# Kernel optimization log

Measured on AMD Instinct MI355X. Metric: run time of the kernel, lower is better.

## Reference

```python
import jax, jax.numpy as jnp
import numpy as np


def setup_inputs() -> dict:
    key = jax.random.key(0)
    k0, k1, k2, k3 = jax.random.split(key, 4)
    B, L, D, H = 8, 4096, 300, 128  # batch, leaves (power of 2), embed dim, hidden
    x = jax.random.normal(k0, (B, L, D), jnp.float32)
    W_leaf = jax.random.normal(k1, (D, 2 * H), jnp.float32) * (1.0 / np.sqrt(D))
    b_leaf = jnp.zeros((2 * H,), jnp.float32)
    W_l = jax.random.normal(k2, (H, 5 * H), jnp.float32) * (1.0 / np.sqrt(H))
    W_r = jax.random.normal(k3, (H, 5 * H), jnp.float32) * (1.0 / np.sqrt(H))
    b = jnp.zeros((5 * H,), jnp.float32)
    return {"x": x, "W_leaf": W_leaf, "b_leaf": b_leaf, "W_l": W_l, "W_r": W_r, "b": b}


def reference(x, W_leaf, b_leaf, W_l, W_r, b):
    """Binary TreeLSTM over a complete tree: leaves -> root.

    x: [B, L, D] leaf embeddings, L a power of 2.
    Leaf transform: linear projection split into (h, c) (SPINN-style).
    REDUCE: 5-gate child-sum-of-two composition.
    Returns root hidden state: [B, H].
    """
    H = W_l.shape[0]
    hc = x @ W_leaf + b_leaf                     # [B, L, 2H]
    h, c = hc[..., :H], hc[..., H:]
    levels = int(np.log2(x.shape[1]))
    for _ in range(levels):                      # level-batched tree reduction
        h_l, h_r = h[:, 0::2], h[:, 1::2]        # [B, n/2, H]
        c_l, c_r = c[:, 0::2], c[:, 1::2]
        gates = h_l @ W_l + h_r @ W_r + b        # [B, n/2, 5H]
        i, fl, fr, o, g = jnp.split(gates, 5, axis=-1)
        c = (jax.nn.sigmoid(fl) * c_l
             + jax.nn.sigmoid(fr) * c_r
             + jax.nn.sigmoid(i) * jnp.tanh(g))
        h = jax.nn.sigmoid(o) * jnp.tanh(c)
    return h[:, 0]                               # root hidden state [B, H]
```

## Files before the change

kernel.cpp:

```cpp
#include <hip/hip_runtime.h>
#include <hip/hip_bf16.h>
#include <math.h>


typedef __attribute__((ext_vector_type(8))) short bfrag8;
typedef __attribute__((ext_vector_type(4))) float f32x4;

__device__ __forceinline__ float rcpf(float x) { return __builtin_amdgcn_rcpf(x); }
__device__ __forceinline__ float sigf(float x) { return rcpf(1.0f + __expf(-x)); }
__device__ __forceinline__ float tanh_f(float x) {
    float e = __expf(2.0f * x);
    return 1.0f - 2.0f * rcpf(e + 1.0f);
}
__device__ __forceinline__ short f2bf(float f) {
    __hip_bfloat16 h = __float2bfloat16(f);
    return *reinterpret_cast<short*>(&h);
}
__device__ __forceinline__ float bf2f(short s) {
    union { unsigned int u; float f; } v;
    v.u = ((unsigned int)(unsigned short)s) << 16;
    return v.f;
}
__device__ __forceinline__ bfrag8 pack8(f32x4 a, f32x4 b) {
    union { int i[4]; bfrag8 v; } u;
    asm("v_cvt_pk_bf16_f32 %0, %1, %2" : "=v"(u.i[0]) : "v"(a[0]), "v"(a[1]));
    asm("v_cvt_pk_bf16_f32 %0, %1, %2" : "=v"(u.i[1]) : "v"(a[2]), "v"(a[3]));
    asm("v_cvt_pk_bf16_f32 %0, %1, %2" : "=v"(u.i[2]) : "v"(b[0]), "v"(b[1]));
    asm("v_cvt_pk_bf16_f32 %0, %1, %2" : "=v"(u.i[3]) : "v"(b[2]), "v"(b[3]));
    return u.v;
}
#define GLDS(gp, lp) __builtin_amdgcn_global_load_lds( \
    (const __attribute__((address_space(1))) void*)(gp), \
    (__attribute__((address_space(3))) void*)(lp), 16, 0, 0)

__global__ __launch_bounds__(256) void leaf_kernel(
    const float* __restrict__ x,     const float* __restrict__ Wleaf,
    const float* __restrict__ W_l,   const float* __restrict__ W_r,
    const float* __restrict__ bleaf,
    short* __restrict__ hD,
    short* __restrict__ cDb,
    short* __restrict__ Wcat_ch)
{
    __shared__ float Als[128 * 64];
    __shared__ short Bls[8 * 256 * 8];
    const int tid  = threadIdx.x;
    const int w    = tid >> 6, lane = tid & 63;
    const int quad = lane >> 4, l16 = lane & 15;
    const int mBlk = blockIdx.x * 128;
    const int waveM = (w >> 1) * 64, waveN = (w & 1) * 64;

    if (blockIdx.x < 160) {
        #pragma unroll
        for (int e = 0; e < 4; ++e) {
            int idx = blockIdx.x * 1024 + e * 256 + tid;
            int n = idx >> 8, k = idx & 255;
            float v = (k < 128) ? W_l[k * 640 + n] : W_r[(k - 128) * 640 + n];
            Wcat_ch[(((size_t)(k >> 3)) * 640 + n) * 8 + (k & 7)] = f2bf(v);
        }
    }

    f32x4 acc[2][4][4] = {};
    const f32x4 zero4 = {0.f, 0.f, 0.f, 0.f};

    for (int c = 0; c < 5; ++c) {
        const int k0c = c * 64;
        {
            const int q_lds = lane & 15;
            const int rsub  = lane >> 4;
            #pragma unroll
            for (int g = 0; g < 8; ++g) {
                int row = w * 32 + g * 4 + rsub;
                int q_g = (q_lds & 8) | ((q_lds & 7) ^ (row & 7));
                if (c < 4 || q_g < 11) {
                    GLDS(x + (size_t)(mBlk + row) * 300 + k0c + q_g * 4,
                         (char*)Als + (w * 32 + g * 4) * 256);
                } else {
                    *(f32x4*)((char*)Als + row * 256 + q_lds * 16) = zero4;
                }
            }
        }
        #pragma unroll
        for (int uu = 0; uu < 8; ++uu) {
            int ccl = uu, nl = tid;
            int k0  = (c * 8 + ccl) * 8;
            f32x4 v0, v1;
            #pragma unroll
            for (int jj = 0; jj < 4; ++jj)
                v0[jj] = (k0 + jj < 300) ? Wleaf[(size_t)(k0 + jj) * 256 + nl] : 0.0f;
            #pragma unroll
            for (int jj = 0; jj < 4; ++jj)
                v1[jj] = (k0 + 4 + jj < 300) ? Wleaf[(size_t)(k0 + 4 + jj) * 256 + nl] : 0.0f;
            *(bfrag8*)(Bls + (ccl * 256 + nl) * 8) = pack8(v0, v1);
        }
        __syncthreads();
        #pragma unroll
        for (int ks = 0; ks < 2; ++ks) {
            const int ca = ks * 4 + quad;
            bfrag8 af[4];
            #pragma unroll
            for (int i = 0; i < 4; ++i) {
                int r  = waveM + i * 16 + l16;
                int u0 = 2 * ca, u1 = 2 * ca + 1;
                int s0 = (u0 & 8) | ((u0 & 7) ^ (r & 7));
                int s1 = (u1 & 8) | ((u1 & 7) ^ (r & 7));
                f32x4 a0 = *(const f32x4*)(Als + r * 64 + s0 * 4);
                f32x4 a1 = *(const f32x4*)(Als + r * 64 + s1 * 4);
                af[i] = pack8(a0, a1);
            }
            #pragma unroll
            for (int nh = 0; nh < 2; ++nh) {
                bfrag8 bf4[4];
                #pragma unroll
                for (int jn = 0; jn < 4; ++jn)
                    bf4[jn] = *(const bfrag8*)(Bls + (ca * 256 + nh * 128
                                                      + waveN + jn * 16 + l16) * 8);
                #pragma unroll
                for (int i = 0; i < 4; ++i)
                    #pragma unroll
                    for (int jn = 0; jn < 4; ++jn)
                        acc[nh][i][jn] = __builtin_amdgcn_mfma_f32_16x16x32_bf16(
                                             af[i], bf4[jn], acc[nh][i][jn], 0, 0, 0);
            }
        }
        __syncthreads();
    }

    #pragma unroll
    for (int nh = 0; nh < 2; ++nh) {
        #pragma unroll
        for (int i = 0; i < 4; ++i) {
            int row0 = mBlk + waveM + i * 16 + quad * 4;
            #pragma unroll
            for (int jn = 0; jn < 4; ++jn) {
                int col = nh * 128 + waveN + jn * 16 + l16;
                float bv = bleaf[col];
                #pragma unroll
                for (int rg = 0; rg < 4; ++rg) {
                    float v = acc[nh][i][jn][rg] + bv;
                    int m = row0 + rg;
                    if (nh == 0) {
                        int hc = col;
                        hD[(((size_t)((m & 1) * 16 + (hc >> 3))) * 16384 + (m >> 1)) * 8
                           + (hc & 7)] = f2bf(v);
                    } else {
                        int ch = col - 128;
                        cDb[(size_t)(ch >> 4) * 32768 * 16 + (size_t)m * 16 + (ch & 15)]
                            = f2bf(v);
                    }
                }
            }
        }
    }
}

template<int CIN_BF, int COUT_BF>
__global__ __launch_bounds__(256, 2) void level_ws_t(
    const short* __restrict__ A,
    const void*  __restrict__ cprev,
    const short* __restrict__ Wch,
    const float* __restrict__ bias,
    short* __restrict__ hout, void* __restrict__ cout_,
    int M, int nst)
{
    __shared__ short Als[32 * 64 * 8];
    const int tid  = threadIdx.x;
    const int w    = tid >> 6, lane = tid & 63;
    const int quad = lane >> 4, l16 = lane & 15;
    const int j   = blockIdx.y;
    const int tb0 = blockIdx.x * 64 * nst;
    const int h   = j * 16 + l16;

    #pragma unroll
    for (int s = 0; s < 8; ++s)
        GLDS(A + ((size_t)(s * 4 + w) * M + tb0 + lane) * 8,
             (char*)Als + (s * 4 + w) * 1024);

    bfrag8 Wfr[5][8];
    #pragma unroll
    for (int g = 0; g < 5; ++g)
        #pragma unroll
        for (int s = 0; s < 8; ++s)
            Wfr[g][s] = *(const bfrag8*)(Wch + ((size_t)(s * 4 + quad) * 640
                                                + g * 128 + h) * 8);
    const float bi  = bias[h],       bfl = bias[128 + h], bfr_ = bias[256 + h];
    const float bo  = bias[384 + h], bg  = bias[512 + h];

    const int Mn = M >> 1;
    for (int st = 0; st < nst; ++st) {
        const int tb = tb0 + st * 64;
        __syncthreads();

        f32x4 acc[5] = {};
        #pragma unroll
        for (int s = 0; s < 8; ++s) {
            bfrag8 af = *(const bfrag8*)(Als + ((s * 4 + quad) * 64 + w * 16 + l16) * 8);
            #pragma unroll
            for (int g = 0; g < 5; ++g)
                acc[g] = __builtin_amdgcn_mfma_f32_16x16x32_bf16(af, Wfr[g][s], acc[g], 0, 0, 0);
        }

        if (st + 1 < nst) {
            __syncthreads();
            #pragma unroll
            for (int s = 0; s < 8; ++s)
                GLDS(A + ((size_t)(s * 4 + w) * M + tb + 64 + lane) * 8,
                     (char*)Als + (s * 4 + w) * 1024);
        }

        #pragma unroll
        for (int rg = 0; rg < 4; ++rg) {
            int m = tb + w * 16 + quad * 4 + rg;
            float gi  = acc[0][rg] + bi;
            float gfl = acc[1][rg] + bfl;
            float gfr = acc[2][rg] + bfr_;
            float go  = acc[3][rg] + bo;
            float gg  = acc[4][rg] + bg;
            float cl, cr;
            if (CIN_BF) {
                const short* cp = (const short*)cprev;
                size_t base = (size_t)(h >> 4) * ((size_t)2 * M) * 16
                              + (size_t)(2 * m) * 16 + (h & 15);
                cl = bf2f(cp[base]);
                cr = bf2f(cp[base + 16]);
            } else {
                const float* cp = (const float*)cprev;
                cl = cp[(size_t)(2 * m) * 128 + h];
                cr = cp[(size_t)(2 * m + 1) * 128 + h];
            }
            float cn  = sigf(gfl) * cl + sigf(gfr) * cr + sigf(gi) * tanh_f(gg);
            float hn  = sigf(go) * tanh_f(cn);
            hout[(((size_t)((m & 1) * 16 + (h >> 3))) * Mn + (m >> 1)) * 8
                 + (h & 7)] = f2bf(hn);
            if (COUT_BF) {
                ((short*)cout_)[(size_t)(h >> 4) * (size_t)M * 16
                                + (size_t)m * 16 + (h & 15)] = f2bf(cn);
            } else {
                ((float*)cout_)[(size_t)m * 128 + h] = cn;
            }
        }
    }
}

__global__ __launch_bounds__(512) void finish_kernel(
    const short* __restrict__ hin,
    const float* __restrict__ cin,
    const short* __restrict__ Wch, const float* __restrict__ bias,
    float* __restrict__ out)
{
    __shared__ short hP[32 * 64 * 8];
    __shared__ short hQ[32 * 32 * 8];
    __shared__ float cA[128 * 128];
    __shared__ float cB[64 * 128];
    const int tid  = threadIdx.x;
    const int w    = tid >> 6, lane = tid & 63;
    const int quad = lane >> 4, l16 = lane & 15;
    const int h    = w * 16 + l16;

    #pragma unroll
    for (int g = 0; g < 4; ++g)
        GLDS(hin + ((size_t)((g * 8 + w) * 64 + lane)) * 8,
             (char*)hP + ((g * 8 + w) * 64) * 16);
    #pragma unroll
    for (int g = 0; g < 8; ++g)
        GLDS(cin + ((size_t)((g * 8 + w) * 64 + lane)) * 4,
             (char*)cA + ((g * 8 + w) * 64) * 16);

    bfrag8 Wfr[5][8];
    #pragma unroll
    for (int g = 0; g < 5; ++g)
        #pragma unroll
        for (int s = 0; s < 8; ++s)
            Wfr[g][s] = *(const bfrag8*)(Wch + ((size_t)(s * 4 + quad) * 640
                                                + g * 128 + h) * 8);
    const float bi  = bias[h],       bfl = bias[128 + h], bfr_ = bias[256 + h];
    const float bo  = bias[384 + h], bg  = bias[512 + h];

    __syncthreads();

    #pragma unroll
    for (int t = 0; t < 4; ++t) {
        const int Mo = 64 >> t;
        const short* hsrc = (t & 1) ? hQ : hP;
        short* hdst       = (t & 1) ? hP : hQ;
        const float* cread  = (t & 1) ? cB : cA;
        float*       cwrite = (t & 1) ? cA : cB;
        const int nrt = (Mo + 15) >> 4;

        for (int rt = 0; rt < nrt; ++rt) {
            f32x4 acc[5] = {};
            #pragma unroll
            for (int s = 0; s < 8; ++s) {
                bfrag8 af = *(const bfrag8*)(hsrc + ((s * 4 + quad) * Mo
                                                     + rt * 16 + l16) * 8);
                #pragma unroll
                for (int g = 0; g < 5; ++g)
                    acc[g] = __builtin_amdgcn_mfma_f32_16x16x32_bf16(
                                 af, Wfr[g][s], acc[g], 0, 0, 0);
            }
            #pragma unroll
            for (int rg = 0; rg < 4; ++rg) {
                int m = rt * 16 + quad * 4 + rg;
                if (m < Mo) {
                    float gi  = acc[0][rg] + bi;
                    float gfl = acc[1][rg] + bfl;
                    float gfr = acc[2][rg] + bfr_;
                    float go  = acc[3][rg] + bo;
                    float gg  = acc[4][rg] + bg;
                    float cl  = cread[(2 * m) * 128 + h];
                    float cr  = cread[(2 * m + 1) * 128 + h];
                    float cn  = sigf(gfl) * cl + sigf(gfr) * cr + sigf(gi) * tanh_f(gg);
                    float hn  = sigf(go) * tanh_f(cn);
                    if (t == 3) {
                        out[(size_t)m * 128 + h] = hn;
                    } else {
                        hdst[(((m & 1) * 16 + (h >> 3)) * (Mo >> 1) + (m >> 1)) * 8
                             + (h & 7)] = f2bf(hn);
                        cwrite[m * 128 + h] = cn;
                    }
                }
            }
        }
        __syncthreads();
    }
}

extern "C" void kernel_launch(void* const* d_in, const int* in_sizes, int n_in,
                              void* d_out, int out_size, void* d_ws, size_t ws_size,
                              hipStream_t stream)
{
    const float* x      = (const float*)d_in[0];
    const float* W_leaf = (const float*)d_in[1];
    const float* b_leaf = (const float*)d_in[2];
    const float* W_l    = (const float*)d_in[3];
    const float* W_r    = (const float*)d_in[4];
    const float* b      = (const float*)d_in[5];
    float* out = (float*)d_out;

    char* p = (char*)d_ws;
    short* hA    = (short*)p; p += (size_t)32 * 16384 * 16 + 1024;
    short* hB    = (short*)p; p += (size_t)32 * 8192 * 16 + 1024;
    char*  c0    = p;         p += (size_t)32768 * 128 * 4;
    char*  c1    = p;         p += (size_t)16384 * 128 * 4;
    short* WcatC = (short*)p; p += (size_t)32 * 640 * 16;

    leaf_kernel<<<256, 256, 0, stream>>>(
        x, W_leaf, W_l, W_r, b_leaf, hA, (short*)c0, WcatC);

    level_ws_t<1, 1><<<dim3(16384 / 256, 8), 256, 0, stream>>>(
        hA, c0, WcatC, b, hB, c1, 16384, 4);
    level_ws_t<1, 0><<<dim3(8192 / 128, 8), 256, 0, stream>>>(
        hB, c1, WcatC, b, hA, c0, 8192, 2);

    const short* hin = hA; const char* cin = c0;
    int M = 4096;
    for (int lev = 3; lev <= 8; ++lev) {
        short* ho = (lev & 1) ? hB : hA;
        char*  co = (lev & 1) ? c1 : c0;
        int nst = (lev == 3) ? 2 : 1;
        level_ws_t<0, 0><<<dim3(M / (64 * nst), 8), 256, 0, stream>>>(
            hin, cin, WcatC, b, ho, co, M, nst);
        hin = ho; cin = co;
        M >>= 1;
    }

    finish_kernel<<<1, 512, 0, stream>>>(hA, (const float*)c0, WcatC, b, out);
}
```

Measured before the change: 167.3 us.

## Pre-convert leaf weights to bf16 in separate kernel and halve leaf tile

Adds a reorder kernel that converts W_l/W_r and W_leaf into bf16 chunked layouts once, instead of every leaf block re-reading fp32 W_leaf with strided scalar loads and converting it. The leaf kernel now streams the pre-packed B tile with async global-to-LDS loads, uses 64-row M tiles with each wave owning 64 columns, and runs 512 blocks for better occupancy. This costs an extra kernel launch and less reuse of each B tile across rows.

Result: no change. 166.2 us (-0.6%).

```diff
diff --git a/kernel.cpp b/kernel.cpp
--- a/kernel.cpp
+++ b/kernel.cpp
@@ -33,33 +33,41 @@
     (const __attribute__((address_space(1))) void*)(gp), \
     (__attribute__((address_space(3))) void*)(lp), 16, 0, 0)
 
+__global__ __launch_bounds__(256) void reorder_kernel(
+    const float* __restrict__ W_l, const float* __restrict__ W_r,
+    const float* __restrict__ W_leaf,
+    short* __restrict__ Wcat_ch, short* __restrict__ Wleaf_ch)
+{
+    int idx = blockIdx.x * 256 + threadIdx.x;
+    if (idx < 163840) {
+        int n = idx >> 8, k = idx & 255;
+        float v = (k < 128) ? W_l[k * 640 + n] : W_r[(k - 128) * 640 + n];
+        Wcat_ch[(((size_t)(k >> 3)) * 640 + n) * 8 + (k & 7)] = f2bf(v);
+        return;
+    }
+    idx -= 163840;
+    if (idx < 81920) {
+        int n = idx / 320, k = idx - n * 320;
+        short v = (k < 300) ? f2bf(W_leaf[k * 256 + n]) : (short)0;
+        Wleaf_ch[(((size_t)(k >> 3)) * 256 + n) * 8 + (k & 7)] = v;
+    }
+}
+
 __global__ __launch_bounds__(256) void leaf_kernel(
-    const float* __restrict__ x,     const float* __restrict__ Wleaf,
-    const float* __restrict__ W_l,   const float* __restrict__ W_r,
+    const float* __restrict__ x,   const short* __restrict__ Bw,
     const float* __restrict__ bleaf,
     short* __restrict__ hD,
-    short* __restrict__ cDb,
-    short* __restrict__ Wcat_ch)
-{
-    __shared__ float Als[128 * 64];
+    short* __restrict__ cDb)
+{
+    __shared__ float Als[64 * 64];
     __shared__ short Bls[8 * 256 * 8];
     const int tid  = threadIdx.x;
     const int w    = tid >> 6, lane = tid & 63;
     const int quad = lane >> 4, l16 = lane & 15;
-    const int mBlk = blockIdx.x * 128;
-    const int waveM = (w >> 1) * 64, waveN = (w & 1) * 64;
-
-    if (blockIdx.x < 160) {
-        #pragma unroll
-        for (int e = 0; e < 4; ++e) {
-            int idx = blockIdx.x * 1024 + e * 256 + tid;
-            int n = idx >> 8, k = idx & 255;
-            float v = (k < 128) ? W_l[k * 640 + n] : W_r[(k - 128) * 640 + n];
-            Wcat_ch[(((size_t)(k >> 3)) * 640 + n) * 8 + (k & 7)] = f2bf(v);
-        }
-    }
-
-    f32x4 acc[2][4][4] = {};
+    const int mBlk = blockIdx.x * 64;
+    const int waveN = w * 64;
+
+    f32x4 acc[4][4] = {};
     const f32x4 zero4 = {0.f, 0.f, 0.f, 0.f};
 
     for (int c = 0; c < 5; ++c) {
@@ -68,38 +76,32 @@
             const int q_lds = lane & 15;
             const int rsub  = lane >> 4;
             #pragma unroll
-            for (int g = 0; g < 8; ++g) {
-                int row = w * 32 + g * 4 + rsub;
+            for (int g = 0; g < 4; ++g) {
+                int row = w * 16 + g * 4 + rsub;
                 int q_g = (q_lds & 8) | ((q_lds & 7) ^ (row & 7));
                 if (c < 4 || q_g < 11) {
                     GLDS(x + (size_t)(mBlk + row) * 300 + k0c + q_g * 4,
-                         (char*)Als + (w * 32 + g * 4) * 256);
+                         (char*)Als + (w * 16 + g * 4) * 256);
                 } else {
                     *(f32x4*)((char*)Als + row * 256 + q_lds * 16) = zero4;
                 }
             }
         }
         #pragma unroll
-        for (int uu = 0; uu < 8; ++uu) {
-            int ccl = uu, nl = tid;
-            int k0  = (c * 8 + ccl) * 8;
-            f32x4 v0, v1;
-            #pragma unroll
-            for (int jj = 0; jj < 4; ++jj)
-                v0[jj] = (k0 + jj < 300) ? Wleaf[(size_t)(k0 + jj) * 256 + nl] : 0.0f;
-            #pragma unroll
-            for (int jj = 0; jj < 4; ++jj)
-                v1[jj] = (k0 + 4 + jj < 300) ? Wleaf[(size_t)(k0 + 4 + jj) * 256 + nl] : 0.0f;
-            *(bfrag8*)(Bls + (ccl * 256 + nl) * 8) = pack8(v0, v1);
+        for (int g = 0; g < 8; ++g) {
+            int i   = w * 8 + g;
+            int cc  = i >> 2, colg = (i & 3) * 64;
+            GLDS(Bw + ((size_t)(c * 8 + cc) * 256 + colg + lane) * 8,
+                 (char*)Bls + ((cc * 256 + colg)) * 16);
         }
         __syncthreads();
         #pragma unroll
         for (int ks = 0; ks < 2; ++ks) {
             const int ca = ks * 4 + quad;
-            bfrag8 af[4];
+            bfrag8 af[4], bf4[4];
             #pragma unroll
             for (int i = 0; i < 4; ++i) {
-                int r  = waveM + i * 16 + l16;
+                int r  = i * 16 + l16;
                 int u0 = 2 * ca, u1 = 2 * ca + 1;
                 int s0 = (u0 & 8) | ((u0 & 7) ^ (r & 7));
                 int s1 = (u1 & 8) | ((u1 & 7) ^ (r & 7));
@@ -108,45 +110,37 @@
                 af[i] = pack8(a0, a1);
             }
             #pragma unroll
-            for (int nh = 0; nh < 2; ++nh) {
-                bfrag8 bf4[4];
+            for (int jn = 0; jn < 4; ++jn)
+                bf4[jn] = *(const bfrag8*)(Bls + (ca * 256 + waveN + jn * 16 + l16) * 8);
+            #pragma unroll
+            for (int i = 0; i < 4; ++i)
                 #pragma unroll
                 for (int jn = 0; jn < 4; ++jn)
-                    bf4[jn] = *(const bfrag8*)(Bls + (ca * 256 + nh * 128
-                                                      + waveN + jn * 16 + l16) * 8);
-                #pragma unroll
-                for (int i = 0; i < 4; ++i)
-                    #pragma unroll
-                    for (int jn = 0; jn < 4; ++jn)
-                        acc[nh][i][jn] = __builtin_amdgcn_mfma_f32_16x16x32_bf16(
-                                             af[i], bf4[jn], acc[nh][i][jn], 0, 0, 0);
-            }
+                    acc[i][jn] = __builtin_amdgcn_mfma_f32_16x16x32_bf16(
+                                     af[i], bf4[jn], acc[i][jn], 0, 0, 0);
         }
         __syncthreads();
     }
 
     #pragma unroll
-    for (int nh = 0; nh < 2; ++nh) {
-        #pragma unroll
-        for (int i = 0; i < 4; ++i) {
-            int row0 = mBlk + waveM + i * 16 + quad * 4;
-            #pragma unroll
-            for (int jn = 0; jn < 4; ++jn) {
-                int col = nh * 128 + waveN + jn * 16 + l16;
-                float bv = bleaf[col];
-                #pragma unroll
-                for (int rg = 0; rg < 4; ++rg) {
-                    float v = acc[nh][i][jn][rg] + bv;
-                    int m = row0 + rg;
-                    if (nh == 0) {
-                        int hc = col;
-                        hD[(((size_t)((m & 1) * 16 + (hc >> 3))) * 16384 + (m >> 1)) * 8
-                           + (hc & 7)] = f2bf(v);
-                    } else {
-                        int ch = col - 128;
-                        cDb[(size_t)(ch >> 4) * 32768 * 16 + (size_t)m * 16 + (ch & 15)]
-                            = f2bf(v);
-                    }
+    for (int i = 0; i < 4; ++i) {
+        int row0 = mBlk + i * 16 + quad * 4;
+        #pragma unroll
+        for (int jn = 0; jn < 4; ++jn) {
+            int col = waveN + jn * 16 + l16;
+            float bv = bleaf[col];
+            #pragma unroll
+            for (int rg = 0; rg < 4; ++rg) {
+                float v = acc[i][jn][rg] + bv;
+                int m = row0 + rg;
+                if (col < 128) {
+                    int hc = col;
+                    hD[(((size_t)((m & 1) * 16 + (hc >> 3))) * 16384 + (m >> 1)) * 8
+                       + (hc & 7)] = f2bf(v);
+                } else {
+                    int ch = col - 128;
+                    cDb[(size_t)(ch >> 4) * 32768 * 16 + (size_t)m * 16 + (ch & 15)]
+                        = f2bf(v);
                 }
             }
         }
@@ -342,9 +336,11 @@
     char*  c0    = p;         p += (size_t)32768 * 128 * 4;
     char*  c1    = p;         p += (size_t)16384 * 128 * 4;
     short* WcatC = (short*)p; p += (size_t)32 * 640 * 16;
-
-    leaf_kernel<<<256, 256, 0, stream>>>(
-        x, W_leaf, W_l, W_r, b_leaf, hA, (short*)c0, WcatC);
+    short* WlfC  = (short*)p; p += (size_t)40 * 256 * 16;
+
+    reorder_kernel<<<960, 256, 0, stream>>>(W_l, W_r, W_leaf, WcatC, WlfC);
+
+    leaf_kernel<<<512, 256, 0, stream>>>(x, WlfC, b_leaf, hA, (short*)c0);
 
     level_ws_t<1, 1><<<dim3(16384 / 256, 8), 256, 0, stream>>>(
         hA, c0, WcatC, b, hB, c1, 16384, 4);
```
